# Kernel tuning notes

Hardware: AMD Instinct MI355X
Metric: run time of the kernel (lower is better)

Reference implementation:

```python
import jax, jax.numpy as jnp
import numpy as np

HEAD_SIZE = 128
N_EMBD = 64
B, T = 8, 4096


def setup_inputs() -> dict:
    key = jax.random.key(0)
    k1, k2, k3, k4 = jax.random.split(key, 4)
    x = jax.random.normal(k1, (B, T, N_EMBD), dtype=jnp.float32)
    Wq = jax.random.normal(k2, (N_EMBD, HEAD_SIZE), dtype=jnp.float32) * (N_EMBD ** -0.5)
    Wk = jax.random.normal(k3, (N_EMBD, HEAD_SIZE), dtype=jnp.float32) * (N_EMBD ** -0.5)
    Wv = jax.random.normal(k4, (N_EMBD, HEAD_SIZE), dtype=jnp.float32) * (N_EMBD ** -0.5)
    return {"x": x, "Wq": Wq, "Wk": Wk, "Wv": Wv}


def reference(x, Wq, Wk, Wv):
    # x: [B, T, C]; single-head causal self-attention (nanoGPT Head)
    q = x @ Wq  # [B, T, H]
    k = x @ Wk  # [B, T, H]
    v = x @ Wv  # [B, T, H]
    scale = HEAD_SIZE ** -0.5
    scores = jnp.einsum("bth,bsh->bts", q, k) * scale  # [B, T, T]
    t = x.shape[1]
    causal = jnp.tril(jnp.ones((t, t), dtype=bool))  # [T, T]
    scores = jnp.where(causal[None, :, :], scores, jnp.float32(-jnp.inf))
    wei = jax.nn.softmax(scores, axis=-1)  # [B, T, T]; dropout p=0.0 -> identity
    out = jnp.einsum("bts,bsh->bth", wei, v)  # [B, T, H]
    return out
```

## Files before the change

kernel.cpp:

```cpp
#include <hip/hip_runtime.h>
#include <math.h>

#define BB 8
#define TT 4096
#define CC 64
#define HH 128
#define NTH 256
#define XSTR 72
#define WSTR 72
#define QSCALE ((float)(0.08838834764831845 * 1.4426950408889634))

typedef __attribute__((ext_vector_type(8)))  short short8;
typedef __attribute__((ext_vector_type(4)))  float floatx4;
typedef __attribute__((ext_vector_type(16))) float floatx16;

__device__ __forceinline__ unsigned short f2bf(float f) {
    union { float f; unsigned int u; } un; un.f = f;
    unsigned int r = un.u + 0x7FFF + ((un.u >> 16) & 1);
    return (unsigned short)(r >> 16);
}
__device__ __forceinline__ unsigned int pack2bf_fast(float a, float b) {
    union { float f; unsigned int u; } ua, ub; ua.f = a; ub.f = b;
    return __builtin_amdgcn_perm(ub.u + 0x8000u, ua.u + 0x8000u, 0x07060302u);
}
__device__ __forceinline__ float bflo(unsigned int u) {
    union { unsigned int u; float f; } x; x.u = u << 16; return x.f;
}
__device__ __forceinline__ float bfhi(unsigned int u) {
    union { unsigned int u; float f; } x; x.u = u & 0xffff0000u; return x.f;
}

__device__ __forceinline__ void gl_lds16(const void* g, void* l) {
    __builtin_amdgcn_global_load_lds(
        (const __attribute__((address_space(1))) unsigned int*)g,
        (__attribute__((address_space(3))) unsigned int*)l, 16, 0, 0);
}

__global__ __launch_bounds__(NTH) void wconv(
    const float* __restrict__ Wq, const float* __restrict__ Wk, const float* __restrict__ Wv,
    unsigned short* __restrict__ Wbf)
{
    const int id = blockIdx.x * NTH + threadIdx.x;
    const int mat = id >> 13;
    const int rem = id & 8191;
    const int h = rem & 127, c = rem >> 7;
    const float* W = mat == 0 ? Wq : (mat == 1 ? Wk : Wv);
    const float s = mat == 0 ? QSCALE : 1.0f;
    Wbf[(mat * HH + h) * WSTR + c] = f2bf(W[c * HH + h] * s);
}

__global__ __launch_bounds__(NTH) void qkv_mfma(
    const float* __restrict__ x, const unsigned short* __restrict__ Wbf,
    unsigned short* __restrict__ qb, unsigned short* __restrict__ Kf,
    unsigned short* __restrict__ Vf)
{
    __shared__ __align__(16) unsigned short xs[64 * XSTR];
    __shared__ __align__(16) unsigned short Wts[3 * HH * WSTR];

    const int tid  = threadIdx.x;
    const int w    = tid >> 6;
    const int lane = tid & 63;
    const int quad = lane >> 4;
    const int lr   = lane & 15;

    const int b    = blockIdx.x >> 6;
    const int kblk = blockIdx.x & 63;
    const int t0   = kblk * 64;
    const long long rbase = (long long)b * TT + t0;

    {
        const unsigned char* ws = (const unsigned char*)Wbf;
        unsigned char* wd = (unsigned char*)Wts;
#pragma unroll
        for (int it = 0; it < 14; ++it) {
            const int off = it * 4096 + tid * 16;
            if (off < 3 * HH * WSTR * 2)
                gl_lds16(ws + off, wd + off);
        }
    }
#pragma unroll
    for (int i = 0; i < 4; ++i) {
        const int idx = tid + i * NTH;
        const int r = idx >> 4, c4 = idx & 15;
        const float4 v = *(const float4*)(x + (rbase + r) * CC + c4 * 4);
        unsigned short tmp[4] = { f2bf(v.x), f2bf(v.y), f2bf(v.z), f2bf(v.w) };
        *(unsigned long long*)&xs[r * XSTR + c4 * 4] = *(unsigned long long*)tmp;
    }
    __syncthreads();

    const short8 bx0 = *(const short8*)&xs[(w * 16 + lr) * XSTR + quad * 8];
    const short8 bx1 = *(const short8*)&xs[(w * 16 + lr) * XSTR + 32 + quad * 8];

    {
        const unsigned short* Wrow = Wts;
#pragma unroll
        for (int ht = 0; ht < 8; ++ht) {
            const short8 aw0 = *(const short8*)(Wrow + (ht * 16 + lr) * WSTR + quad * 8);
            const short8 aw1 = *(const short8*)(Wrow + (ht * 16 + lr) * WSTR + 32 + quad * 8);
            floatx4 acc = (floatx4)0.f;
            acc = __builtin_amdgcn_mfma_f32_16x16x32_bf16(aw0, bx0, acc, 0, 0, 0);
            acc = __builtin_amdgcn_mfma_f32_16x16x32_bf16(aw1, bx1, acc, 0, 0, 0);
            ushort4 st = { f2bf(acc[0]), f2bf(acc[1]), f2bf(acc[2]), f2bf(acc[3]) };
            *(ushort4*)(qb + (rbase + w * 16 + lr) * HH + ht * 16 + quad * 4) = st;
        }
    }
    {
        const unsigned short* Wrow = Wts + 1 * HH * WSTR;
        const int khp = w >> 1;
        const int lqp = (w & 1) * 16 + lr;
        unsigned short* kdst = Kf + ((long long)((b * 64 + kblk) * 2 + khp)) * 4096
                             + ((quad >> 1) & 1) * 256 + lqp * 8 + (quad & 1) * 4;
#pragma unroll
        for (int ht = 0; ht < 8; ++ht) {
            const short8 aw0 = *(const short8*)(Wrow + (ht * 16 + lr) * WSTR + quad * 8);
            const short8 aw1 = *(const short8*)(Wrow + (ht * 16 + lr) * WSTR + 32 + quad * 8);
            floatx4 acc = (floatx4)0.f;
            acc = __builtin_amdgcn_mfma_f32_16x16x32_bf16(aw0, bx0, acc, 0, 0, 0);
            acc = __builtin_amdgcn_mfma_f32_16x16x32_bf16(aw1, bx1, acc, 0, 0, 0);
            ushort4 st = { f2bf(acc[0]), f2bf(acc[1]), f2bf(acc[2]), f2bf(acc[3]) };
            *(ushort4*)(kdst + ht * 512) = st;
        }
    }
    {
        const unsigned short* Wrow = Wts + 2 * HH * WSTR;
        const int khv = w >> 1, ksv = w & 1, lsv = (quad >> 1) & 1;
        unsigned short* vdst = Vf + (long long)(b * 64 + kblk) * 8192 + khv * 4096
                             + ksv * 512 + lsv * 256 + (quad & 1) * 4;
#pragma unroll
        for (int htp = 0; htp < 8; ++htp) {
            const short8 bw0 = *(const short8*)(Wrow + (htp * 16 + lr) * WSTR + quad * 8);
            const short8 bw1 = *(const short8*)(Wrow + (htp * 16 + lr) * WSTR + 32 + quad * 8);
            floatx4 acc = (floatx4)0.f;
            acc = __builtin_amdgcn_mfma_f32_16x16x32_bf16(bx0, bw0, acc, 0, 0, 0);
            acc = __builtin_amdgcn_mfma_f32_16x16x32_bf16(bx1, bw1, acc, 0, 0, 0);
            ushort4 st = { f2bf(acc[0]), f2bf(acc[1]), f2bf(acc[2]), f2bf(acc[3]) };
            *(ushort4*)(vdst + (htp >> 1) * 1024 + ((htp & 1) * 16 + lr) * 8) = st;
        }
    }
}

__device__ __forceinline__ void dma_tile32(
    const unsigned char* __restrict__ Kj, const unsigned char* __restrict__ Vj,
    unsigned char* buf, int w, int lane)
{
    const unsigned char* src;
    unsigned char* dst;
    if (w < 2) { src = Kj + w * 4096 + lane * 16;        dst = buf + w * 4096; }
    else       { src = Vj + (w - 2) * 4096 + lane * 16;  dst = buf + 8192 + (w - 2) * 4096; }
#pragma unroll
    for (int i = 0; i < 4; ++i)
        gl_lds16(src + i * 1024, dst + i * 1024);
}

__global__ __launch_bounds__(NTH, 3) void flash_splitk(
    const unsigned short* __restrict__ qb,
    const unsigned short* __restrict__ Kf,
    const unsigned short* __restrict__ Vf,
    unsigned short* __restrict__ Ob, float* __restrict__ Lb)
{
    __shared__ __align__(16) unsigned char KV[2][16384];

    const int tid  = threadIdx.x;
    const int w    = tid >> 6;
    const int lane = tid & 63;
    const int lq   = lane & 31;
    const int ls   = lane >> 5;

    const int id = blockIdx.x;
    const int b  = id & 7;
    const int c  = (id >> 3) & 3;
    const int qt = 31 - (id >> 5);
    const int len = qt + 1;
    const int lo  = c * len;
    const int hi  = lo + qt;

    const int q0 = qt * 128;
    const long long baset = (long long)b * TT;
    const unsigned char* Kbase = (const unsigned char*)Kf + (long long)b * 128 * 8192;
    const unsigned char* Vbase = (const unsigned char*)Vf + (long long)b * 128 * 8192;

    dma_tile32(Kbase + (long long)lo * 8192, Vbase + (long long)lo * 8192, KV[0], w, lane);

    short8 aq[8];
    {
        const unsigned short* qrp = qb + (baset + q0 + w * 32 + lq) * HH + ls * 8;
#pragma unroll
        for (int st = 0; st < 8; ++st)
            aq[st] = *(const short8*)(qrp + st * 16);
    }

    floatx16 o_acc[4];
#pragma unroll
    for (int ht = 0; ht < 4; ++ht) o_acc[ht] = (floatx16)0.f;
    float l_lane = 0.f;

    for (int j = lo; j <= hi; ++j) {
        const int cb = (j - lo) & 1;
        __syncthreads();
        if (j < hi)
            dma_tile32(Kbase + (long long)(j + 1) * 8192, Vbase + (long long)(j + 1) * 8192,
                       KV[cb ^ 1], w, lane);

        const int D = q0 + w * 32 - j * 32;
        if (D > -32) {
            const unsigned short* Kt = (const unsigned short*)&KV[cb][0];
            const unsigned short* Vt = (const unsigned short*)&KV[cb][8192];

            short8 kfr[8], vfr[8];
#pragma unroll
            for (int st = 0; st < 8; ++st)
                kfr[st] = *(const short8*)(Kt + st * 512 + lane * 8);
#pragma unroll
            for (int i = 0; i < 8; ++i)
                vfr[i] = *(const short8*)(Vt + (i >> 1) * 1024 + (i & 1) * 512 + lane * 8);

            floatx16 s_acc = (floatx16)0.f;
#pragma unroll
            for (int st = 0; st < 8; ++st)
                s_acc = __builtin_amdgcn_mfma_f32_32x32x16_bf16(kfr[st], aq[st], s_acc, 0, 0, 0);

            float p[16];
            if (D < 31) {
#pragma unroll
                for (int reg = 0; reg < 16; ++reg) {
                    const int kk = (reg & 3) + 8 * (reg >> 2) + 4 * ls;
                    p[reg] = (kk <= lq + D) ? __builtin_amdgcn_exp2f(s_acc[reg]) : 0.f;
                }
            } else {
#pragma unroll
                for (int reg = 0; reg < 16; ++reg)
                    p[reg] = __builtin_amdgcn_exp2f(s_acc[reg]);
            }
#pragma unroll
            for (int reg = 0; reg < 16; ++reg) l_lane += p[reg];

            unsigned int g[8], pg[8];
#pragma unroll
            for (int i = 0; i < 8; ++i) g[i] = pack2bf_fast(p[2 * i], p[2 * i + 1]);
#pragma unroll
            for (int i = 0; i < 8; ++i) pg[i] = __shfl_xor((int)g[i], 32);
            short8 bp[2];
#pragma unroll
            for (int ks = 0; ks < 2; ++ks) {
                union { short8 s; unsigned int u[4]; } fr;
                const int bs = ks * 4;
                if (ls == 0) {
                    fr.u[0] = g[bs];      fr.u[1] = g[bs + 1];
                    fr.u[2] = pg[bs];     fr.u[3] = pg[bs + 1];
                } else {
                    fr.u[0] = pg[bs + 2]; fr.u[1] = pg[bs + 3];
                    fr.u[2] = g[bs + 2];  fr.u[3] = g[bs + 3];
                }
                bp[ks] = fr.s;
            }

#pragma unroll
            for (int ht = 0; ht < 4; ++ht) {
                o_acc[ht] = __builtin_amdgcn_mfma_f32_32x32x16_bf16(vfr[ht * 2 + 0], bp[0], o_acc[ht], 0, 0, 0);
                o_acc[ht] = __builtin_amdgcn_mfma_f32_32x32x16_bf16(vfr[ht * 2 + 1], bp[1], o_acc[ht], 0, 0, 0);
            }
        }
    }

    const int pid = ((b * 32 + qt) << 2) + c;
    const float l2 = l_lane + __shfl_xor(l_lane, 32);
    if (lane < 32) Lb[pid * 128 + w * 32 + lq] = l2;

    unsigned short* od = Ob + (long long)pid * 16384 + (w * 32 + lq) * HH;
#pragma unroll
    for (int ht = 0; ht < 4; ++ht)
#pragma unroll
        for (int rg = 0; rg < 4; ++rg) {
            uint2 st;
            st.x = pack2bf_fast(o_acc[ht][rg * 4 + 0], o_acc[ht][rg * 4 + 1]);
            st.y = pack2bf_fast(o_acc[ht][rg * 4 + 2], o_acc[ht][rg * 4 + 3]);
            *(uint2*)(od + ht * 32 + rg * 8 + 4 * ls) = st;
        }
}

__global__ __launch_bounds__(NTH) void combine(
    const unsigned short* __restrict__ Ob, const float* __restrict__ Lb,
    float* __restrict__ out)
{
    const int id = blockIdx.x;
    const int b = id & 7;
    const int rest = id >> 3;
    const int qt = rest >> 1, half = rest & 1;
    const int tid = threadIdx.x;
    const int q = half * 64 + (tid >> 2);
    const int hg = tid & 3;
    const int pid0 = ((b * 32 + qt) << 2);

    float acc[32];
#pragma unroll
    for (int i = 0; i < 32; ++i) acc[i] = 0.f;
    float ltot = 0.f;

#pragma unroll
    for (int c = 0; c < 4; ++c) {
        ltot += Lb[(pid0 + c) * 128 + q];
        const uint4* src = (const uint4*)(Ob + (long long)(pid0 + c) * 16384 + q * HH + hg * 32);
#pragma unroll
        for (int g = 0; g < 4; ++g) {
            const uint4 d = src[g];
            acc[g * 8 + 0] += bflo(d.x); acc[g * 8 + 1] += bfhi(d.x);
            acc[g * 8 + 2] += bflo(d.y); acc[g * 8 + 3] += bfhi(d.y);
            acc[g * 8 + 4] += bflo(d.z); acc[g * 8 + 5] += bfhi(d.z);
            acc[g * 8 + 6] += bflo(d.w); acc[g * 8 + 7] += bfhi(d.w);
        }
    }
    const float inv = 1.f / ltot;
    float* op = out + ((long long)b * TT + qt * 128 + q) * HH + hg * 32;
#pragma unroll
    for (int g = 0; g < 8; ++g) {
        float4 st = make_float4(acc[g * 4 + 0] * inv, acc[g * 4 + 1] * inv,
                                acc[g * 4 + 2] * inv, acc[g * 4 + 3] * inv);
        *(float4*)(op + g * 4) = st;
    }
}

extern "C" void kernel_launch(void* const* d_in, const int* in_sizes, int n_in,
                              void* d_out, int out_size, void* d_ws, size_t ws_size,
                              hipStream_t stream)
{
    const float* x  = (const float*)d_in[0];
    const float* Wq = (const float*)d_in[1];
    const float* Wk = (const float*)d_in[2];
    const float* Wv = (const float*)d_in[3];
    float* out = (float*)d_out;

    const long long n = (long long)BB * TT * HH;
    unsigned short* qb = (unsigned short*)d_ws;
    unsigned short* Kf = qb + n;
    unsigned short* Vf = Kf + n;
    unsigned short* Ob = Vf + n;
    float*          Lb = (float*)(Ob + (long long)1024 * 16384);
    unsigned short* Wbf = (unsigned short*)(Lb + 1024 * 128);

    wconv<<<96, NTH, 0, stream>>>(Wq, Wk, Wv, Wbf);
    qkv_mfma<<<BB * (TT / 64), NTH, 0, stream>>>(x, Wbf, qb, Kf, Vf);
    flash_splitk<<<1024, NTH, 0, stream>>>(qb, Kf, Vf, Ob, Lb);
    combine<<<BB * 64, NTH, 0, stream>>>(Ob, Lb, out);
}
```

Baseline: 141.5 us.

## Fuse split-K combine into flash kernel via per-tile atomic arrival counter

Removes the separate combine kernel launch. Each split-K block increments a per-tile counter after writing its partial output and row sums, and the last block to arrive for a tile does the reduction and writes the final fp32 output. The counters are zeroed in the weight-conversion kernel. This saves a launch and the gap between kernels, and lets combine work overlap with remaining flash blocks. The cost is fences and atomics, plus a serial tail of work on whichever block arrives last.

```diff
diff --git a/kernel.cpp b/kernel.cpp
--- a/kernel.cpp
+++ b/kernel.cpp
@@ -38,9 +38,11 @@
 
 __global__ __launch_bounds__(NTH) void wconv(
     const float* __restrict__ Wq, const float* __restrict__ Wk, const float* __restrict__ Wv,
-    unsigned short* __restrict__ Wbf)
-{
-    const int id = blockIdx.x * NTH + threadIdx.x;
+    unsigned short* __restrict__ Wbf, int* __restrict__ Cnt)
+{
+    const int tid = threadIdx.x;
+    if (blockIdx.x == 0) Cnt[tid] = 0;
+    const int id = blockIdx.x * NTH + tid;
     const int mat = id >> 13;
     const int rem = id & 8191;
     const int h = rem & 127, c = rem >> 7;
@@ -156,9 +158,11 @@
     const unsigned short* __restrict__ qb,
     const unsigned short* __restrict__ Kf,
     const unsigned short* __restrict__ Vf,
-    unsigned short* __restrict__ Ob, float* __restrict__ Lb)
+    unsigned short* __restrict__ Ob, float* __restrict__ Lb,
+    int* __restrict__ Cnt, float* __restrict__ out)
 {
     __shared__ __align__(16) unsigned char KV[2][16384];
+    __shared__ int sArr;
 
     const int tid  = threadIdx.x;
     const int w    = tid >> 6;
@@ -262,7 +266,8 @@
         }
     }
 
-    const int pid = ((b * 32 + qt) << 2) + c;
+    const int tile = b * 32 + qt;
+    const int pid = (tile << 2) + c;
     const float l2 = l_lane + __shfl_xor(l_lane, 32);
     if (lane < 32) Lb[pid * 128 + w * 32 + lq] = l2;
 
@@ -276,46 +281,46 @@
             st.y = pack2bf_fast(o_acc[ht][rg * 4 + 2], o_acc[ht][rg * 4 + 3]);
             *(uint2*)(od + ht * 32 + rg * 8 + 4 * ls) = st;
         }
-}
-
-__global__ __launch_bounds__(NTH) void combine(
-    const unsigned short* __restrict__ Ob, const float* __restrict__ Lb,
-    float* __restrict__ out)
-{
-    const int id = blockIdx.x;
-    const int b = id & 7;
-    const int rest = id >> 3;
-    const int qt = rest >> 1, half = rest & 1;
-    const int tid = threadIdx.x;
-    const int q = half * 64 + (tid >> 2);
-    const int hg = tid & 3;
-    const int pid0 = ((b * 32 + qt) << 2);
-
-    float acc[32];
-#pragma unroll
-    for (int i = 0; i < 32; ++i) acc[i] = 0.f;
-    float ltot = 0.f;
-
-#pragma unroll
-    for (int c = 0; c < 4; ++c) {
-        ltot += Lb[(pid0 + c) * 128 + q];
-        const uint4* src = (const uint4*)(Ob + (long long)(pid0 + c) * 16384 + q * HH + hg * 32);
-#pragma unroll
-        for (int g = 0; g < 4; ++g) {
-            const uint4 d = src[g];
-            acc[g * 8 + 0] += bflo(d.x); acc[g * 8 + 1] += bfhi(d.x);
-            acc[g * 8 + 2] += bflo(d.y); acc[g * 8 + 3] += bfhi(d.y);
-            acc[g * 8 + 4] += bflo(d.z); acc[g * 8 + 5] += bfhi(d.z);
-            acc[g * 8 + 6] += bflo(d.w); acc[g * 8 + 7] += bfhi(d.w);
-        }
-    }
-    const float inv = 1.f / ltot;
-    float* op = out + ((long long)b * TT + qt * 128 + q) * HH + hg * 32;
-#pragma unroll
-    for (int g = 0; g < 8; ++g) {
-        float4 st = make_float4(acc[g * 4 + 0] * inv, acc[g * 4 + 1] * inv,
-                                acc[g * 4 + 2] * inv, acc[g * 4 + 3] * inv);
-        *(float4*)(op + g * 4) = st;
+
+    __syncthreads();
+    if (tid == 0) {
+        __threadfence();
+        sArr = atomicAdd(&Cnt[tile], 1);
+    }
+    __syncthreads();
+    if (sArr == 3) {
+        __threadfence();
+        const int pid0 = tile << 2;
+        const int hg = tid & 3;
+#pragma unroll
+        for (int pass = 0; pass < 2; ++pass) {
+            const int q = pass * 64 + (tid >> 2);
+            float acc[32];
+#pragma unroll
+            for (int i = 0; i < 32; ++i) acc[i] = 0.f;
+            float ltot = 0.f;
+#pragma unroll
+            for (int cc = 0; cc < 4; ++cc) {
+                ltot += Lb[(pid0 + cc) * 128 + q];
+                const uint4* src = (const uint4*)(Ob + (long long)(pid0 + cc) * 16384 + q * HH + hg * 32);
+#pragma unroll
+                for (int g = 0; g < 4; ++g) {
+                    const uint4 d = src[g];
+                    acc[g * 8 + 0] += bflo(d.x); acc[g * 8 + 1] += bfhi(d.x);
+                    acc[g * 8 + 2] += bflo(d.y); acc[g * 8 + 3] += bfhi(d.y);
+                    acc[g * 8 + 4] += bflo(d.z); acc[g * 8 + 5] += bfhi(d.z);
+                    acc[g * 8 + 6] += bflo(d.w); acc[g * 8 + 7] += bfhi(d.w);
+                }
+            }
+            const float inv = 1.f / ltot;
+            float* op = out + (baset + q0 + q) * HH + hg * 32;
+#pragma unroll
+            for (int g = 0; g < 8; ++g) {
+                float4 st = make_float4(acc[g * 4 + 0] * inv, acc[g * 4 + 1] * inv,
+                                        acc[g * 4 + 2] * inv, acc[g * 4 + 3] * inv);
+                *(float4*)(op + g * 4) = st;
+            }
+        }
     }
 }
 
@@ -336,9 +341,9 @@
     unsigned short* Ob = Vf + n;
     float*          Lb = (float*)(Ob + (long long)1024 * 16384);
     unsigned short* Wbf = (unsigned short*)(Lb + 1024 * 128);
-
-    wconv<<<96, NTH, 0, stream>>>(Wq, Wk, Wv, Wbf);
+    int*            Cnt = (int*)(Wbf + 3 * HH * WSTR);
+
+    wconv<<<96, NTH, 0, stream>>>(Wq, Wk, Wv, Wbf, Cnt);
     qkv_mfma<<<BB * (TT / 64), NTH, 0, stream>>>(x, Wbf, qb, Kf, Vf);
-    flash_splitk<<<1024, NTH, 0, stream>>>(qb, Kf, Vf, Ob, Lb);
-    combine<<<BB * 64, NTH, 0, stream>>>(Ob, Lb, out);
-}
+    flash_splitk<<<1024, NTH, 0, stream>>>(qb, Kf, Vf, Ob, Lb, Cnt, out);
+}
```

Result: slower. 238.4 us (+68.4%).
